# Kernel tuning notes

Measured on AMD Instinct MI355X. Metric: run time of the kernel, lower is better.

The kernel has to match this reference:

```python
import jax, jax.numpy as jnp
import numpy as np

D = 4096      # hidden_size
H = 32        # num_attention_heads
DH = 128      # head_dim
DR = 64       # rope_head_dim (rotated suffix of head_dim)
G = 4         # o_groups
QLR = 1536    # q_lora_rank
OLR = 512     # o_lora_rank
WIN = 2048    # window_size
EPS = 1e-6    # norm_eps
THETA = 10000.0


def rms_norm(x, g):
    return x * jax.lax.rsqrt(jnp.mean(x * x, axis=-1, keepdims=True) + EPS) * g


def rope_interleave(x, cos, sin):
    # interleaved (non-neox) rotary: pairs are adjacent even/odd lanes
    x0, x1 = x[..., 0::2], x[..., 1::2]
    r0 = x0 * cos - x1 * sin
    r1 = x0 * sin + x1 * cos
    return jnp.stack([r0, r1], axis=-1).reshape(x.shape)


def setup_inputs() -> dict:
    ks = jax.random.split(jax.random.key(0), 9)
    B, S = 1, 2048
    return {
        "hidden_states": jax.random.normal(ks[0], (B, S, D), jnp.float32),
        "positions": jnp.arange(S, dtype=jnp.int64),
        "wq_a": jax.random.normal(ks[1], (QLR, D), jnp.float32) * 0.02,
        "q_norm_g": jnp.ones((QLR,), jnp.float32),
        "wq_b": jax.random.normal(ks[2], (H * DH, QLR), jnp.float32) * 0.02,
        "wkv": jax.random.normal(ks[3], (DH, D), jnp.float32) * 0.02,
        "kv_norm_g": jnp.ones((DH,), jnp.float32),
        "wo_a": jax.random.normal(ks[4], (G, OLR, (H * DH) // G), jnp.float32) * 0.02,
        "wo_b": jax.random.normal(ks[5], (D, G * OLR), jnp.float32) * 0.02,
        "attn_sink": jax.random.normal(ks[6], (H,), jnp.float32),
    }


def reference(hidden_states, positions, wq_a, q_norm_g, wq_b, wkv, kv_norm_g, wo_a, wo_b, attn_sink):
    B, S, _ = hidden_states.shape
    # low-rank Q path: wq_a -> RMSNorm -> wq_b -> [B,S,H,DH]
    qr = rms_norm(hidden_states @ wq_a.T, q_norm_g)
    q = (qr @ wq_b.T).reshape(B, S, H, DH)
    # shared latent KV (single head_dim vector, MLA/MQA style): wkv -> RMSNorm
    kv = rms_norm(hidden_states @ wkv.T, kv_norm_g)  # [B,S,DH]
    # rotary tables (interleave mode)
    inv_freq = 1.0 / (THETA ** (jnp.arange(0, DR, 2, dtype=jnp.float32) / DR))
    ang = positions.astype(jnp.float32)[:, None] * inv_freq  # [S, DR/2]
    cos, sin = jnp.cos(ang), jnp.sin(ang)
    # rotate last DR dims of q and k
    q = jnp.concatenate(
        [q[..., : DH - DR], rope_interleave(q[..., DH - DR :], cos[None, :, None, :], sin[None, :, None, :])], -1)
    k = jnp.concatenate(
        [kv[..., : DH - DR], rope_interleave(kv[..., DH - DR :], cos[None, :, :], sin[None, :, :])], -1)
    # windowed causal attention with learned per-head sink logit
    scores = jnp.einsum("bshd,btd->bhst", q, k) * (DH ** -0.5)  # [B,H,S,S]
    i = jnp.arange(S)[:, None]
    j = jnp.arange(S)[None, :]
    mask = (j <= i) & ((i - j) < WIN)
    scores = jnp.where(mask[None, None], scores, jnp.finfo(scores.dtype).min)
    sink = jnp.broadcast_to(attn_sink[None, :, None, None], (B, H, S, 1))
    probs = jax.nn.softmax(jnp.concatenate([scores, sink], axis=-1), axis=-1)[..., :S]
    # value = shared normalized latent (pre-rope)
    out = jnp.einsum("bhst,btd->bshd", probs, kv)  # [B,S,H,DH]
    # grouped low-rank output projection: wo_a per group, then wo_b
    out = out.reshape(B, S, G, (H * DH) // G)
    low = jnp.einsum("bsgd,gkd->bsgk", out, wo_a).reshape(B, S, G * OLR)
    return low @ wo_b.T
```

## Files before the change

kernel.cpp:

```cpp
#include <hip/hip_runtime.h>

typedef unsigned short u16;
typedef __bf16 bf16x8 __attribute__((ext_vector_type(8)));
typedef float  f32x4  __attribute__((ext_vector_type(4)));

#define EPSF 1e-6f

__device__ __forceinline__ u16 f2b(float f) {
  unsigned u = __float_as_uint(f);
  u += 0x7fffu + ((u >> 16) & 1u);
  return (u16)(u >> 16);
}
__device__ __forceinline__ float b2f(u16 u) { return __uint_as_float(((unsigned)u) << 16); }

__device__ __forceinline__ void dma16(const u16* g, u16* l) {
  __builtin_amdgcn_global_load_lds(
      (const __attribute__((address_space(1))) unsigned int*)g,
      (__attribute__((address_space(3))) unsigned int*)l, 16, 0, 0);
}

__global__ void dsv4_cvt(const float* __restrict__ hidden, const float* __restrict__ wq_a,
                         const float* __restrict__ wq_b, const float* __restrict__ wkv,
                         const float* __restrict__ wo_a, const float* __restrict__ wo_b,
                         u16* hb, u16* qab, u16* qbb, u16* kvb, u16* oab, u16* obb)
{
  long c = (long)blockIdx.x * 256 + threadIdx.x;
  const float* s; u16* d; long off;
  if      (c < 1048576) { s = hidden; d = hb;  off = c; }
  else if (c < 1835008) { s = wq_a;   d = qab; off = c - 1048576; }
  else if (c < 2621440) { s = wq_b;   d = qbb; off = c - 1835008; }
  else if (c < 2686976) { s = wkv;    d = kvb; off = c - 2621440; }
  else if (c < 2949120) { s = wo_a;   d = oab; off = c - 2686976; }
  else                  { s = wo_b;   d = obb; off = c - 2949120; }
  const float* p = s + off * 8;
  float4 f0 = *(const float4*)p;
  float4 f1 = *(const float4*)(p + 4);
  union { u16 h[8]; int4 v; } u;
  u.h[0] = f2b(f0.x); u.h[1] = f2b(f0.y); u.h[2] = f2b(f0.z); u.h[3] = f2b(f0.w);
  u.h[4] = f2b(f1.x); u.h[5] = f2b(f1.y); u.h[6] = f2b(f1.z); u.h[7] = f2b(f1.w);
  *(int4*)(d + off * 8) = u.v;
}

template<int BM, bool C_F32>
__global__ __launch_bounds__(256, 2)
void dsv4_gemm(const u16* __restrict__ A, int lda, long sAz,
               const u16* __restrict__ B, int ldb, long sBz,
               void* __restrict__ Cv, int ldc, long sCz,
               int K, int splitTile,
               const u16* __restrict__ Baux, void* __restrict__ Caux, int ldcAux)
{
  constexpr int AI = (BM * 4) / 256;
  constexpr int NJ = (BM == 128) ? 4 : 2;
  __shared__ __align__(16) u16 As[BM * 32];
  __shared__ __align__(16) u16 Bs[128 * 32];

  const int tid   = threadIdx.x;
  const int lane  = tid & 63;
  const int q     = lane >> 4;
  const int l16   = lane & 15;
  const int wid   = tid >> 6;
  const int wbase = tid & 192;

  int n0 = blockIdx.x * 128;
  const int m0 = blockIdx.y * BM;
  void* Cp = Cv;
  if ((int)blockIdx.x >= splitTile) {
    B = Baux; Cp = Caux; ldc = ldcAux;
    n0 = ((int)blockIdx.x - splitTile) * 128;
  }
  A += (long)blockIdx.z * sAz;
  B += (long)blockIdx.z * sBz;

  const u16* gA[AI]; u16* lA[AI];
#pragma unroll
  for (int j = 0; j < AI; j++) {
    int L = j * 256 + tid, row = L >> 2, c = (L & 3) ^ ((row >> 1) & 3);
    gA[j] = A + (long)(m0 + row) * lda + c * 8;
    lA[j] = As + (j * 256 + wbase) * 8;
  }
  const u16* gB[2]; u16* lB[2];
#pragma unroll
  for (int j = 0; j < 2; j++) {
    int L = j * 256 + tid, row = L >> 2, c = (L & 3) ^ ((row >> 1) & 3);
    gB[j] = B + (long)(n0 + row) * ldb + c * 8;
    lB[j] = Bs + (j * 256 + wbase) * 8;
  }

  f32x4 acc[4][NJ];
#pragma unroll
  for (int i = 0; i < 4; i++)
#pragma unroll
    for (int j = 0; j < NJ; j++) { f32x4 z = {0.f, 0.f, 0.f, 0.f}; acc[i][j] = z; }

  const int wm = (BM == 128) ? (wid >> 1) * 64 : 0;
  const int wn = (BM == 128) ? (wid & 1) * 64 : wid * 32;

  for (int k0 = 0; k0 < K; k0 += 32) {
    __syncthreads();
#pragma unroll
    for (int j = 0; j < AI; j++) dma16(gA[j] + k0, lA[j]);
#pragma unroll
    for (int j = 0; j < 2; j++)  dma16(gB[j] + k0, lB[j]);
    asm volatile("s_waitcnt vmcnt(0)" ::: "memory");
    __syncthreads();

    bf16x8 af[4], bg[NJ];
#pragma unroll
    for (int i = 0; i < 4; i++) {
      int row = wm + i * 16 + l16;
      af[i] = *(const bf16x8*)&As[row * 32 + ((q ^ ((row >> 1) & 3)) << 3)];
    }
#pragma unroll
    for (int j = 0; j < NJ; j++) {
      int row = wn + j * 16 + l16;
      bg[j] = *(const bf16x8*)&Bs[row * 32 + ((q ^ ((row >> 1) & 3)) << 3)];
    }
#pragma unroll
    for (int i = 0; i < 4; i++)
#pragma unroll
      for (int j = 0; j < NJ; j++)
        acc[i][j] = __builtin_amdgcn_mfma_f32_16x16x32_bf16(af[i], bg[j], acc[i][j], 0, 0, 0);
  }

#pragma unroll
  for (int i = 0; i < 4; i++)
#pragma unroll
    for (int j = 0; j < NJ; j++)
#pragma unroll
      for (int rr = 0; rr < 4; rr++) {
        long row = m0 + wm + i * 16 + q * 4 + rr;
        int  col = n0 + wn + j * 16 + l16;
        if (C_F32)
          ((float*)Cp)[row * ldc + col + (long)blockIdx.z * sCz] = acc[i][j][rr];
        else
          ((u16*)Cp)[row * ldc + col + (long)blockIdx.z * sCz] = f2b(acc[i][j][rr]);
      }
}

__global__ void dsv4_rmsnorm(const u16* __restrict__ X, const float* __restrict__ g,
                             u16* __restrict__ Y, int W, float invW)
{
  __shared__ float wsum[4];
  const int row = blockIdx.x;
  const u16* x = X + (long)row * W;
  u16* y = Y + (long)row * W;
  float ss = 0.f;
  for (int i = threadIdx.x; i < W; i += 256) { float v = b2f(x[i]); ss += v * v; }
#pragma unroll
  for (int o = 32; o > 0; o >>= 1) ss += __shfl_xor(ss, o);
  const int wid = threadIdx.x >> 6;
  if ((threadIdx.x & 63) == 0) wsum[wid] = ss;
  __syncthreads();
  float tot = wsum[0] + wsum[1] + wsum[2] + wsum[3];
  float scale = rsqrtf(tot * invW + EPSF);
  for (int i = threadIdx.x; i < W; i += 256)
    y[i] = f2b(b2f(x[i]) * scale * g[i]);
}

__global__ void dsv4_kv_finalize(const u16* __restrict__ KVp, const float* __restrict__ g,
                                 u16* __restrict__ Kout, u16* __restrict__ VTout)
{
  const int wid  = threadIdx.x >> 6;
  const int lane = threadIdx.x & 63;
  const int row  = blockIdx.x * 4 + wid;
  const u16* x = KVp + (long)row * 128;
  float x0 = b2f(x[2 * lane]);
  float x1 = b2f(x[2 * lane + 1]);
  float ss = x0 * x0 + x1 * x1;
#pragma unroll
  for (int o = 32; o > 0; o >>= 1) ss += __shfl_xor(ss, o);
  float scale = rsqrtf(ss * (1.f / 128.f) + EPSF);
  float v0 = x0 * scale * g[2 * lane];
  float v1 = x1 * scale * g[2 * lane + 1];
  VTout[(long)(2 * lane) * 2048 + row]     = f2b(v0);
  VTout[(long)(2 * lane + 1) * 2048 + row] = f2b(v1);
  float k0 = v0, k1 = v1;
  if (lane >= 32) {
    int i = lane - 32;
    float invf = powf(10000.f, -(float)i * (1.f / 32.f));
    float sn, cc;
    sincosf((float)row * invf, &sn, &cc);
    k0 = v0 * cc - v1 * sn;
    k1 = v0 * sn + v1 * cc;
  }
  Kout[(long)row * 128 + 2 * lane]     = f2b(k0);
  Kout[(long)row * 128 + 2 * lane + 1] = f2b(k1);
}

__device__ __forceinline__ void attn_step(
    const bf16x8* qf, bool diag, const u16* __restrict__ KsB,
    const u16* __restrict__ VsB, u16* __restrict__ PsW,
    int w, int qd, int l16, int swz, float* m, float* l, f32x4* o)
{
  const float scl2 = 0.12754245006257017f;
  f32x4 st[4];
#pragma unroll
  for (int i = 0; i < 4; i++) { f32x4 z = {0.f, 0.f, 0.f, 0.f}; st[i] = z; }
#pragma unroll
  for (int ks = 0; ks < 4; ks++) {
#pragma unroll
    for (int nt = 0; nt < 4; nt++) {
      int row = nt * 16 + l16;
      bf16x8 bk = *(const bf16x8*)&KsB[row * 128 + ((((ks << 2) + qd) ^ swz) << 3)];
      st[nt] = __builtin_amdgcn_mfma_f32_16x16x32_bf16(qf[ks], bk, st[nt], 0, 0, 0);
    }
  }

#pragma unroll
  for (int nt = 0; nt < 4; nt++)
#pragma unroll
    for (int rr = 0; rr < 4; rr++) {
      float v = st[nt][rr] * scl2;
      if (diag && (nt * 16 + l16) > (w * 16 + qd * 4 + rr)) v = -3.0e38f;
      st[nt][rr] = v;
    }

  float alpha[4];
#pragma unroll
  for (int rr = 0; rr < 4; rr++) {
    float tm = fmaxf(fmaxf(st[0][rr], st[1][rr]), fmaxf(st[2][rr], st[3][rr]));
    tm = fmaxf(tm, __shfl_xor(tm, 1));
    tm = fmaxf(tm, __shfl_xor(tm, 2));
    tm = fmaxf(tm, __shfl_xor(tm, 4));
    tm = fmaxf(tm, __shfl_xor(tm, 8));
    float mnew = fmaxf(m[rr], tm);
    alpha[rr] = exp2f(m[rr] - mnew);
    m[rr] = mnew;
  }
#pragma unroll
  for (int nt = 0; nt < 4; nt++)
#pragma unroll
    for (int rr = 0; rr < 4; rr++)
      st[nt][rr] = exp2f(st[nt][rr] - m[rr]);
#pragma unroll
  for (int rr = 0; rr < 4; rr++) {
    float rs = st[0][rr] + st[1][rr] + st[2][rr] + st[3][rr];
    rs += __shfl_xor(rs, 1);
    rs += __shfl_xor(rs, 2);
    rs += __shfl_xor(rs, 4);
    rs += __shfl_xor(rs, 8);
    l[rr] = l[rr] * alpha[rr] + rs;
  }
#pragma unroll
  for (int nt = 0; nt < 8; nt++)
#pragma unroll
    for (int rr = 0; rr < 4; rr++)
      o[nt][rr] *= alpha[rr];

#pragma unroll
  for (int nt = 0; nt < 4; nt++)
#pragma unroll
    for (int rr = 0; rr < 4; rr++) {
      int row = qd * 4 + rr;
      int cl2 = ((nt << 1) + (l16 >> 3)) ^ (row & 7);
      PsW[row * 64 + (cl2 << 3) + (l16 & 7)] = f2b(st[nt][rr]);
    }
  asm volatile("s_waitcnt lgkmcnt(0)" ::: "memory");

#pragma unroll
  for (int ks = 0; ks < 2; ks++) {
    bf16x8 ap = *(const bf16x8*)&PsW[l16 * 64 + ((((ks << 2) + qd) ^ swz) << 3)];
#pragma unroll
    for (int nt = 0; nt < 8; nt++) {
      int row = nt * 16 + l16;
      bf16x8 bv = *(const bf16x8*)&VsB[row * 64 + ((((ks << 2) + qd) ^ swz) << 3)];
      o[nt] = __builtin_amdgcn_mfma_f32_16x16x32_bf16(ap, bv, o[nt], 0, 0, 0);
    }
  }
}

__global__ __launch_bounds__(256, 2)
void dsv4_attn(const u16* __restrict__ Q, const u16* __restrict__ Km,
               const u16* __restrict__ VT, const float* __restrict__ sinkp,
               u16* __restrict__ O)
{
  __shared__ __align__(16) u16 Ks[2][64 * 128];
  __shared__ __align__(16) u16 Vs[2][128 * 64];
  __shared__ __align__(16) u16 Ps[4][16 * 64];

  const int b  = blockIdx.x;
  const int h  = blockIdx.y;
  const int qtA = 31 - b, qtB = b;
  const int n1 = qtA + 1, nT = n1 + qtB + 1;
  const int tid  = threadIdx.x;
  const int lane = tid & 63;
  const int w    = tid >> 6;
  const int qd   = lane >> 4;
  const int l16  = lane & 15;
  const int swz  = l16 & 7;

  bf16x8 qfA[4], qfB[4];
#pragma unroll
  for (int t = 0; t < 2; t++) {
    int srow = (t ? qtB : qtA) * 64 + w * 16 + l16;
    const u16* qp = Q + (long)srow * 4096 + h * 128 + qd * 8;
    bf16x8* qf = t ? qfB : qfA;
#pragma unroll
    for (int ks = 0; ks < 4; ks++) {
      union { int4 v; u16 hh[8]; } u;
      u.v = *(const int4*)(qp + ks * 32);
      if (ks >= 2) {
#pragma unroll
        for (int j = 0; j < 4; j++) {
          int i = (ks - 2) * 16 + qd * 4 + j;
          float invf = exp2f((float)i * (-13.287712379549449f / 32.f));
          float sn, cc;
          sincosf((float)srow * invf, &sn, &cc);
          float x0 = b2f(u.hh[2 * j]), x1 = b2f(u.hh[2 * j + 1]);
          u.hh[2 * j]     = f2b(x0 * cc - x1 * sn);
          u.hh[2 * j + 1] = f2b(x0 * sn + x1 * cc);
        }
      }
      qf[ks] = *(bf16x8*)&u;
    }
  }

  const u16* gK[4]; const u16* gV[4]; int lKo[4], lVo[4];
#pragma unroll
  for (int j = 0; j < 4; j++) {
    int cl = j * 256 + tid;
    int krow = cl >> 4, kc = (cl & 15) ^ (krow & 7);
    gK[j] = Km + (long)krow * 128 + kc * 8;
    lKo[j] = (j * 256 + (tid & 192)) * 8;
    int vrow = cl >> 3, vc = (cl & 7) ^ (vrow & 7);
    gV[j] = VT + (long)vrow * 2048 + vc * 8;
    lVo[j] = (j * 256 + (tid & 192)) * 8;
  }

  float m[4], l[4];
  f32x4 o[8];
#pragma unroll
  for (int i = 0; i < 4; i++) { m[i] = -INFINITY; l[i] = 0.f; }
#pragma unroll
  for (int i = 0; i < 8; i++) { f32x4 z = {0.f, 0.f, 0.f, 0.f}; o[i] = z; }

  const float sink2 = sinkp[h] * 1.4426950408889634f;

#pragma unroll
  for (int j = 0; j < 4; j++) { dma16(gK[j], &Ks[0][lKo[j]]); dma16(gV[j], &Vs[0][lVo[j]]); }

  for (int it = 0; it < nT; ++it) {
    int nxt = it + 1;
    if (nxt < nT) {
      int kt2 = (nxt < n1) ? nxt : nxt - n1;
      int pb = nxt & 1;
#pragma unroll
      for (int j = 0; j < 4; j++) {
        dma16(gK[j] + (long)kt2 * 8192, &Ks[pb][lKo[j]]);
        dma16(gV[j] + (long)kt2 * 64,   &Vs[pb][lVo[j]]);
      }
    }
    asm volatile("s_waitcnt vmcnt(8)" ::: "memory");
    asm volatile("s_barrier" ::: "memory");
    const int cb = it & 1;

    if (it < n1)
      attn_step(qfA, it == n1 - 1, Ks[cb], Vs[cb], Ps[w], w, qd, l16, swz, m, l, o);
    else
      attn_step(qfB, it == nT - 1, Ks[cb], Vs[cb], Ps[w], w, qd, l16, swz, m, l, o);

    asm volatile("s_barrier" ::: "memory");

    if (it == n1 - 1) {
      float inv[4];
#pragma unroll
      for (int rr = 0; rr < 4; rr++) inv[rr] = 1.f / (l[rr] + exp2f(sink2 - m[rr]));
#pragma unroll
      for (int nt = 0; nt < 8; nt++)
#pragma unroll
        for (int rr = 0; rr < 4; rr++)
          O[(long)(qtA * 64 + w * 16 + qd * 4 + rr) * 4096 + h * 128 + nt * 16 + l16] =
              f2b(o[nt][rr] * inv[rr]);
#pragma unroll
      for (int i = 0; i < 4; i++) { m[i] = -INFINITY; l[i] = 0.f; }
#pragma unroll
      for (int i = 0; i < 8; i++) { f32x4 z = {0.f, 0.f, 0.f, 0.f}; o[i] = z; }
    }
  }

  float inv[4];
#pragma unroll
  for (int rr = 0; rr < 4; rr++) inv[rr] = 1.f / (l[rr] + exp2f(sink2 - m[rr]));
#pragma unroll
  for (int nt = 0; nt < 8; nt++)
#pragma unroll
    for (int rr = 0; rr < 4; rr++)
      O[(long)(qtB * 64 + w * 16 + qd * 4 + rr) * 4096 + h * 128 + nt * 16 + l16] =
          f2b(o[nt][rr] * inv[rr]);
}

extern "C" void kernel_launch(void* const* d_in, const int* in_sizes, int n_in,
                              void* d_out, int out_size, void* d_ws, size_t ws_size,
                              hipStream_t stream)
{
  (void)in_sizes; (void)n_in; (void)out_size; (void)ws_size;
  const float* hidden = (const float*)d_in[0];
  const float* wq_a  = (const float*)d_in[2];
  const float* q_g   = (const float*)d_in[3];
  const float* wq_b  = (const float*)d_in[4];
  const float* wkv   = (const float*)d_in[5];
  const float* kv_g  = (const float*)d_in[6];
  const float* wo_a  = (const float*)d_in[7];
  const float* wo_b  = (const float*)d_in[8];
  const float* sinkp = (const float*)d_in[9];
  float* out = (float*)d_out;

  char* ws = (char*)d_ws;
  u16* hb     = (u16*)(ws);
  u16* low    = (u16*)(ws);
  u16* qab    = (u16*)(ws + (17ul << 20));
  u16* qr     = (u16*)(ws + (17ul << 20));
  u16* qbb    = (u16*)(ws + (30ul << 20));
  u16* kvb    = (u16*)(ws + (43ul << 20));
  u16* oab    = (u16*)(ws + (45ul << 20));
  u16* obb    = (u16*)(ws + (50ul << 20));
  u16* qbuf   = (u16*)(ws + (67ul << 20));
  u16* attnout= (u16*)(ws + (84ul << 20));
  u16* qr_pre = (u16*)(ws + (101ul << 20));
  u16* kvpre  = (u16*)(ws + (108ul << 20));
  u16* kmat   = (u16*)(ws + (108ul << 20) + 524288u);
  u16* vt     = (u16*)(ws + (108ul << 20) + 1048576u);

  const int BIG = 1 << 29;
  dim3 blk(256);

  dsv4_cvt<<<15616, blk, 0, stream>>>(hidden, wq_a, wq_b, wkv, wo_a, wo_b,
                                      hb, qab, qbb, kvb, oab, obb);
  dsv4_gemm<64, false><<<dim3(13, 32, 1), blk, 0, stream>>>(
      hb, 4096, 0, qab, 4096, 0, qr_pre, 1536, 0, 4096, 12, kvb, kvpre, 128);
  dsv4_rmsnorm<<<2048, blk, 0, stream>>>(qr_pre, q_g, qr, 1536, 1.f / 1536.f);
  dsv4_kv_finalize<<<512, blk, 0, stream>>>(kvpre, kv_g, kmat, vt);
  dsv4_gemm<128, false><<<dim3(32, 16, 1), blk, 0, stream>>>(
      qr, 1536, 0, qbb, 1536, 0, qbuf, 4096, 0, 1536, BIG, nullptr, nullptr, 0);
  dsv4_attn<<<dim3(16, 32, 1), blk, 0, stream>>>(qbuf, kmat, vt, sinkp, attnout);
  dsv4_gemm<64, false><<<dim3(4, 32, 4), blk, 0, stream>>>(
      attnout, 4096, 1024, oab, 1024, 524288, low, 2048, 512, 1024, BIG,
      nullptr, nullptr, 0);
  dsv4_gemm<128, true><<<dim3(32, 16, 1), blk, 0, stream>>>(
      low, 2048, 0, obb, 2048, 0, out, 4096, 0, 2048, BIG, nullptr, nullptr, 0);
}
```

Before: 452.7 us.

## Lazy softmax rescaling, deferred row-sum reduction, and MFMA priority hints in attention

Reworks the online softmax in the attention inner step. The running max is now updated only when a tile's max exceeds it by more than a threshold, so the exp rescale of O and l is usually skipped. Scale and max-subtract are fused into one fma before exp2, and the per-row sum is kept per lane, with the cross-lane shuffle reduction done once at finalization. It also wraps the MFMA loops in s_setprio and uses the hardware bf16 convert. The risk is larger unnormalized exponents, up to 2^62 times the true scale, which leaves less fp32 and bf16 headroom.

```diff
diff --git a/kernel.cpp b/kernel.cpp
--- a/kernel.cpp
+++ b/kernel.cpp
@@ -12,6 +12,7 @@
   return (u16)(u >> 16);
 }
 __device__ __forceinline__ float b2f(u16 u) { return __uint_as_float(((unsigned)u) << 16); }
+__device__ __forceinline__ u16 f2bh(float f) { return __builtin_bit_cast(u16, (__bf16)f); }
 
 __device__ __forceinline__ void dma16(const u16* g, u16* l) {
   __builtin_amdgcn_global_load_lds(
@@ -190,12 +191,15 @@
 __device__ __forceinline__ void attn_step(
     const bf16x8* qf, bool diag, const u16* __restrict__ KsB,
     const u16* __restrict__ VsB, u16* __restrict__ PsW,
-    int w, int qd, int l16, int swz, float* m, float* l, f32x4* o)
+    int w, int qd, int l16, int swz, float* m, float* negm, float* l, f32x4* o)
 {
   const float scl2 = 0.12754245006257017f;
+  const float THRU = 62.0f;
   f32x4 st[4];
 #pragma unroll
   for (int i = 0; i < 4; i++) { f32x4 z = {0.f, 0.f, 0.f, 0.f}; st[i] = z; }
+
+  __builtin_amdgcn_s_setprio(1);
 #pragma unroll
   for (int ks = 0; ks < 4; ks++) {
 #pragma unroll
@@ -205,58 +209,53 @@
       st[nt] = __builtin_amdgcn_mfma_f32_16x16x32_bf16(qf[ks], bk, st[nt], 0, 0, 0);
     }
   }
+  __builtin_amdgcn_s_setprio(0);
+
+  if (diag) {
+#pragma unroll
+    for (int nt = 0; nt < 4; nt++)
+#pragma unroll
+      for (int rr = 0; rr < 4; rr++)
+        if ((nt * 16 + l16) > (w * 16 + qd * 4 + rr)) st[nt][rr] = -3.0e38f;
+  }
+
+  float tm[4];
+  bool need = false;
+#pragma unroll
+  for (int rr = 0; rr < 4; rr++) {
+    float t = fmaxf(fmaxf(st[0][rr], st[1][rr]), fmaxf(st[2][rr], st[3][rr]));
+    t = fmaxf(t, __shfl_xor(t, 1));
+    t = fmaxf(t, __shfl_xor(t, 2));
+    t = fmaxf(t, __shfl_xor(t, 4));
+    t = fmaxf(t, __shfl_xor(t, 8));
+    tm[rr] = t;
+    need = need || (t > m[rr] + THRU);
+  }
+  if (__any(need)) {
+#pragma unroll
+    for (int rr = 0; rr < 4; rr++) {
+      float mn = fmaxf(m[rr], tm[rr]);
+      float a  = exp2f(scl2 * (m[rr] - mn));
+      m[rr] = mn; negm[rr] = -scl2 * mn;
+      l[rr] *= a;
+#pragma unroll
+      for (int nt = 0; nt < 8; nt++) o[nt][rr] *= a;
+    }
+  }
 
 #pragma unroll
   for (int nt = 0; nt < 4; nt++)
 #pragma unroll
     for (int rr = 0; rr < 4; rr++) {
-      float v = st[nt][rr] * scl2;
-      if (diag && (nt * 16 + l16) > (w * 16 + qd * 4 + rr)) v = -3.0e38f;
-      st[nt][rr] = v;
-    }
-
-  float alpha[4];
-#pragma unroll
-  for (int rr = 0; rr < 4; rr++) {
-    float tm = fmaxf(fmaxf(st[0][rr], st[1][rr]), fmaxf(st[2][rr], st[3][rr]));
-    tm = fmaxf(tm, __shfl_xor(tm, 1));
-    tm = fmaxf(tm, __shfl_xor(tm, 2));
-    tm = fmaxf(tm, __shfl_xor(tm, 4));
-    tm = fmaxf(tm, __shfl_xor(tm, 8));
-    float mnew = fmaxf(m[rr], tm);
-    alpha[rr] = exp2f(m[rr] - mnew);
-    m[rr] = mnew;
-  }
-#pragma unroll
-  for (int nt = 0; nt < 4; nt++)
-#pragma unroll
-    for (int rr = 0; rr < 4; rr++)
-      st[nt][rr] = exp2f(st[nt][rr] - m[rr]);
-#pragma unroll
-  for (int rr = 0; rr < 4; rr++) {
-    float rs = st[0][rr] + st[1][rr] + st[2][rr] + st[3][rr];
-    rs += __shfl_xor(rs, 1);
-    rs += __shfl_xor(rs, 2);
-    rs += __shfl_xor(rs, 4);
-    rs += __shfl_xor(rs, 8);
-    l[rr] = l[rr] * alpha[rr] + rs;
-  }
-#pragma unroll
-  for (int nt = 0; nt < 8; nt++)
-#pragma unroll
-    for (int rr = 0; rr < 4; rr++)
-      o[nt][rr] *= alpha[rr];
-
-#pragma unroll
-  for (int nt = 0; nt < 4; nt++)
-#pragma unroll
-    for (int rr = 0; rr < 4; rr++) {
+      float p = exp2f(fmaf(st[nt][rr], scl2, negm[rr]));
+      l[rr] += p;
       int row = qd * 4 + rr;
       int cl2 = ((nt << 1) + (l16 >> 3)) ^ (row & 7);
-      PsW[row * 64 + (cl2 << 3) + (l16 & 7)] = f2b(st[nt][rr]);
+      PsW[row * 64 + (cl2 << 3) + (l16 & 7)] = f2bh(p);
     }
   asm volatile("s_waitcnt lgkmcnt(0)" ::: "memory");
 
+  __builtin_amdgcn_s_setprio(1);
 #pragma unroll
   for (int ks = 0; ks < 2; ks++) {
     bf16x8 ap = *(const bf16x8*)&PsW[l16 * 64 + ((((ks << 2) + qd) ^ swz) << 3)];
@@ -267,6 +266,7 @@
       o[nt] = __builtin_amdgcn_mfma_f32_16x16x32_bf16(ap, bv, o[nt], 0, 0, 0);
     }
   }
+  __builtin_amdgcn_s_setprio(0);
 }
 
 __global__ __launch_bounds__(256, 2)
@@ -327,10 +327,10 @@
     lVo[j] = (j * 256 + (tid & 192)) * 8;
   }
 
-  float m[4], l[4];
+  float m[4], negm[4], l[4];
   f32x4 o[8];
 #pragma unroll
-  for (int i = 0; i < 4; i++) { m[i] = -INFINITY; l[i] = 0.f; }
+  for (int i = 0; i < 4; i++) { m[i] = -INFINITY; negm[i] = 0.f; l[i] = 0.f; }
 #pragma unroll
   for (int i = 0; i < 8; i++) { f32x4 z = {0.f, 0.f, 0.f, 0.f}; o[i] = z; }
 
@@ -355,24 +355,31 @@
     const int cb = it & 1;
 
     if (it < n1)
-      attn_step(qfA, it == n1 - 1, Ks[cb], Vs[cb], Ps[w], w, qd, l16, swz, m, l, o);
+      attn_step(qfA, it == n1 - 1, Ks[cb], Vs[cb], Ps[w], w, qd, l16, swz, m, negm, l, o);
     else
-      attn_step(qfB, it == nT - 1, Ks[cb], Vs[cb], Ps[w], w, qd, l16, swz, m, l, o);
+      attn_step(qfB, it == nT - 1, Ks[cb], Vs[cb], Ps[w], w, qd, l16, swz, m, negm, l, o);
 
     asm volatile("s_barrier" ::: "memory");
 
     if (it == n1 - 1) {
       float inv[4];
 #pragma unroll
-      for (int rr = 0; rr < 4; rr++) inv[rr] = 1.f / (l[rr] + exp2f(sink2 - m[rr]));
+      for (int rr = 0; rr < 4; rr++) {
+        float ls = l[rr];
+        ls += __shfl_xor(ls, 1);
+        ls += __shfl_xor(ls, 2);
+        ls += __shfl_xor(ls, 4);
+        ls += __shfl_xor(ls, 8);
+        inv[rr] = 1.f / (ls + exp2f(sink2 + negm[rr]));
+      }
 #pragma unroll
       for (int nt = 0; nt < 8; nt++)
 #pragma unroll
         for (int rr = 0; rr < 4; rr++)
           O[(long)(qtA * 64 + w * 16 + qd * 4 + rr) * 4096 + h * 128 + nt * 16 + l16] =
-              f2b(o[nt][rr] * inv[rr]);
-#pragma unroll
-      for (int i = 0; i < 4; i++) { m[i] = -INFINITY; l[i] = 0.f; }
+              f2bh(o[nt][rr] * inv[rr]);
+#pragma unroll
+      for (int i = 0; i < 4; i++) { m[i] = -INFINITY; negm[i] = 0.f; l[i] = 0.f; }
 #pragma unroll
       for (int i = 0; i < 8; i++) { f32x4 z = {0.f, 0.f, 0.f, 0.f}; o[i] = z; }
     }
@@ -380,13 +387,20 @@
 
   float inv[4];
 #pragma unroll
-  for (int rr = 0; rr < 4; rr++) inv[rr] = 1.f / (l[rr] + exp2f(sink2 - m[rr]));
+  for (int rr = 0; rr < 4; rr++) {
+    float ls = l[rr];
+    ls += __shfl_xor(ls, 1);
+    ls += __shfl_xor(ls, 2);
+    ls += __shfl_xor(ls, 4);
+    ls += __shfl_xor(ls, 8);
+    inv[rr] = 1.f / (ls + exp2f(sink2 + negm[rr]));
+  }
 #pragma unroll
   for (int nt = 0; nt < 8; nt++)
 #pragma unroll
     for (int rr = 0; rr < 4; rr++)
       O[(long)(qtB * 64 + w * 16 + qd * 4 + rr) * 4096 + h * 128 + nt * 16 + l16] =
-          f2b(o[nt][rr] * inv[rr]);
+          f2bh(o[nt][rr] * inv[rr]);
 }
 
 extern "C" void kernel_launch(void* const* d_in, const int* in_sizes, int n_in,
```

After: 440.8 us. 2.6% less time.
